# Performance work log

Measured on AMD Instinct MI355X. Metric: run time of the kernel, lower is better.

The kernel has to match this reference:

```python
import jax, jax.numpy as jnp
import numpy as np

EPS = 1e-6


def _layernorm2d(x, w, b):
    # Normalize over channel dim (axis=1) per pixel; x: [B,C,H,W]
    mu = jnp.mean(x, axis=1, keepdims=True)
    var = jnp.var(x, axis=1, keepdims=True)
    xn = (x - mu) * jax.lax.rsqrt(var + EPS)
    return xn * w[None, :, None, None] + b[None, :, None, None]


def _conv1x1(x, w, b):
    # 1x1 conv == channel matmul; w: [Cout, Cin], x: [B,Cin,H,W]
    return jnp.einsum('oc,bchw->bohw', w, x) + b[None, :, None, None]


def setup_inputs() -> dict:
    key = jax.random.key(0)
    ks = jax.random.split(key, 8)
    B, C, H, W = 4, 64, 180, 320
    s = C ** -0.5  # keep projection weights at sane scale
    return {
        'x_l': jax.random.normal(ks[0], (B, C, H, W), jnp.float32),
        'x_r': jax.random.normal(ks[1], (B, C, H, W), jnp.float32),
        'ln_l_w': jnp.ones((C,), jnp.float32),
        'ln_l_b': jnp.zeros((C,), jnp.float32),
        'ln_r_w': jnp.ones((C,), jnp.float32),
        'ln_r_b': jnp.zeros((C,), jnp.float32),
        'wq_l': jax.random.normal(ks[2], (C, C), jnp.float32) * s,
        'bq_l': jnp.zeros((C,), jnp.float32),
        'wq_r': jax.random.normal(ks[3], (C, C), jnp.float32) * s,
        'bq_r': jnp.zeros((C,), jnp.float32),
        'wv_l': jax.random.normal(ks[4], (C, C), jnp.float32) * s,
        'bv_l': jnp.zeros((C,), jnp.float32),
        'wv_r': jax.random.normal(ks[5], (C, C), jnp.float32) * s,
        'bv_r': jnp.zeros((C,), jnp.float32),
        'beta': jax.random.normal(ks[6], (C,), jnp.float32) * 0.1,
        'gamma': jax.random.normal(ks[7], (C,), jnp.float32) * 0.1,
    }


def reference(x_l, x_r, ln_l_w, ln_l_b, ln_r_w, ln_r_b,
              wq_l, bq_l, wq_r, bq_r, wv_l, bv_l, wv_r, bv_r,
              beta, gamma):
    C = x_l.shape[1]
    scale = C ** -0.5
    # Q projections of LayerNorm'd inputs (Select stub == identity pass-through)
    Q_l = _conv1x1(_layernorm2d(x_l, ln_l_w, ln_l_b), wq_l, bq_l)  # [B,C,H,W]
    Q_r = _conv1x1(_layernorm2d(x_r, ln_r_w, ln_r_b), wq_r, bq_r)  # [B,C,H,W]
    V_l = _conv1x1(x_l, wv_l, bv_l)  # [B,C,H,W]
    V_r = _conv1x1(x_r, wv_r, bv_r)  # [B,C,H,W]
    # attention over width per row: [B,H,Wl,Wr]
    attn = jnp.einsum('bchw,bchv->bhwv', Q_l, Q_r) * scale
    # r -> l: softmax over Wr (last axis), contract with V_r
    F_r2l = jnp.einsum('bhwv,bchv->bchw', jax.nn.softmax(attn, axis=-1), V_r)
    # l -> r: softmax over Wl (axis=2 of attn), contract with V_l
    F_l2r = jnp.einsum('bhwv,bchw->bchv', jax.nn.softmax(attn, axis=2), V_l)
    out_l = x_l + F_r2l * beta[None, :, None, None]
    out_r = x_r + F_l2r * gamma[None, :, None, None]
    return (out_l, out_r)
```

## Files before the change

### kernel.cpp

```cpp
#include <hip/hip_runtime.h>


#define HWs  57600
#define CHWs 3686400
#define TOTs 14745600
#define RST  72
#define VST  328
#define PTS  40

typedef short bf16x8 __attribute__((ext_vector_type(8)));
typedef float f32x4  __attribute__((ext_vector_type(4)));
union FragU { uint4 q; unsigned short u[8]; bf16x8 v; };

__device__ __forceinline__ unsigned short f2bf(float f) {
  unsigned u = __float_as_uint(f);
  u += 0x7fffu + ((u >> 16) & 1u);
  return (unsigned short)(u >> 16);
}
__device__ __forceinline__ float bf2f(unsigned short s) {
  return __uint_as_float(((unsigned)s) << 16);
}

__global__ __launch_bounds__(512, 2) void sfam_kernel(
    const float* __restrict__ x_l, const float* __restrict__ x_r,
    const float* __restrict__ ln_l_w, const float* __restrict__ ln_l_b,
    const float* __restrict__ ln_r_w, const float* __restrict__ ln_r_b,
    const float* __restrict__ wq_l, const float* __restrict__ bq_l,
    const float* __restrict__ wq_r, const float* __restrict__ bq_r,
    const float* __restrict__ wv_l, const float* __restrict__ bv_l,
    const float* __restrict__ wv_r, const float* __restrict__ bv_r,
    const float* __restrict__ beta, const float* __restrict__ gamma,
    float* __restrict__ out)
{
  __shared__ __align__(16) unsigned short Rs[320*RST];
  __shared__ __align__(16) unsigned short Ks[320*RST];
  __shared__ __align__(16) unsigned short Vb[64*VST];
  __shared__ __align__(16) unsigned short Pt[8*16*PTS];
  __shared__ float SR[8*320];
  __shared__ float MU[640], RSd[640];
  __shared__ float c_arr[320];
  __shared__ float BB[128];

  const int bh = blockIdx.x;
  const int b = bh / 180, h = bh - b*180;
  const int base = b*CHWs + h*320;

  const int t = threadIdx.x;
  const int wave = t >> 6, lane = t & 63;
  const int p = lane & 15, g = lane >> 4;
  const int nwt = (wave < 4) ? 3 : 2;
  const int w0 = (wave < 4) ? wave*48 : 192 + (wave-4)*32;

  for (int idx = t; idx < 1280; idx += 512) {
    int r2 = idx; const int side = (r2 >= 640); r2 -= side*640;
    const int half = (r2 >= 320); const int w = r2 - half*320;
    const int cb = half*32;
    const float* xp = side ? x_r : x_l;
    unsigned short* dst = side ? Ks : Rs;
    float s = 0.f, q = 0.f;
    #pragma unroll 8
    for (int c = 0; c < 32; ++c) {
      float v = xp[base + (cb+c)*HWs + w];
      s += v; q += v*v;
      dst[w*RST + cb + c] = f2bf(v);
    }
    SR[(side*2+half)*320 + w] = s;
    SR[(4+side*2+half)*320 + w] = q;
  }
  if (t < 128) {
    const int o = t & 63;
    const float* wqp = (t < 64) ? wq_l : wq_r;
    const float* lwp = (t < 64) ? ln_l_w : ln_r_w;
    const float* lbp = (t < 64) ? ln_l_b : ln_r_b;
    const float* bqp = (t < 64) ? bq_l : bq_r;
    float s = bqp[o];
    for (int c = 0; c < 64; ++c) s += wqp[o*64+c]*lwp[c]*lbp[c];
    BB[t] = s;
  }
  __syncthreads();
  for (int i = t; i < 640; i += 512) {
    const int side = (i >= 320); const int w = i - side*320;
    float m = (SR[(side*2)*320+w] + SR[(side*2+1)*320+w]) * (1.f/64.f);
    float q = (SR[(4+side*2)*320+w] + SR[(4+side*2+1)*320+w]) * (1.f/64.f) - m*m;
    MU[i] = m;
    RSd[i] = rsqrtf(q + 1e-6f);
  }
  __syncthreads();

  auto projV = [&](const float* wvp, const float* bvp, const unsigned short* src,
                   const float* mup, const float* rsp, bool inv) {
    bf16x8 bx[3][2];
    #pragma unroll
    for (int nt = 0; nt < 3; ++nt) if (nt < nwt) {
      const int w = w0 + nt*16 + p;
      const float mu = mup[w];
      const float sd = inv ? (1.0f / rsp[w]) : 0.f;
      #pragma unroll
      for (int kf = 0; kf < 2; ++kf) {
        FragU f; f.q = *(const uint4*)&src[w*RST + kf*32 + g*8];
        if (inv) {
          FragU rr;
          #pragma unroll
          for (int j = 0; j < 8; ++j) rr.u[j] = f2bf(bf2f(f.u[j])*sd + mu);
          bx[nt][kf] = rr.v;
        } else bx[nt][kf] = f.v;
      }
    }
    bf16x8 av[4][2];
    #pragma unroll
    for (int mt = 0; mt < 4; ++mt)
      #pragma unroll
      for (int kf = 0; kf < 2; ++kf) {
        FragU rr;
        #pragma unroll
        for (int j = 0; j < 8; ++j) rr.u[j] = f2bf(wvp[(mt*16+p)*64 + kf*32 + g*8 + j]);
        av[mt][kf] = rr.v;
      }
    f32x4 acc[4][3];
    #pragma unroll
    for (int mt = 0; mt < 4; ++mt)
      #pragma unroll
      for (int nt = 0; nt < 3; ++nt) acc[mt][nt] = (f32x4){0.f,0.f,0.f,0.f};
    #pragma unroll
    for (int mt = 0; mt < 4; ++mt)
      #pragma unroll
      for (int nt = 0; nt < 3; ++nt) if (nt < nwt)
        #pragma unroll
        for (int kf = 0; kf < 2; ++kf)
          acc[mt][nt] = __builtin_amdgcn_mfma_f32_16x16x32_bf16(av[mt][kf], bx[nt][kf], acc[mt][nt], 0,0,0);
    #pragma unroll
    for (int mt = 0; mt < 4; ++mt)
      #pragma unroll
      for (int nt = 0; nt < 3; ++nt) if (nt < nwt)
        #pragma unroll
        for (int r = 0; r < 4; ++r) {
          const int o = mt*16 + g*4 + r;
          Vb[o*VST + w0 + nt*16 + p] = f2bf(acc[mt][nt][r] + bvp[o]);
        }
  };

  projV(wv_l, bv_l, Rs, MU, RSd, false);

  float cR[3][4];
  {
    bf16x8 qa[3][2];
    #pragma unroll
    for (int wt = 0; wt < 3; ++wt) if (wt < nwt) {
      const int w = w0 + wt*16 + p;
      const float mu = MU[w], rs = RSd[w];
      #pragma unroll
      for (int kf = 0; kf < 2; ++kf) {
        FragU f; f.q = *(const uint4*)&Rs[w*RST + kf*32 + g*8];
        FragU rr;
        #pragma unroll
        for (int j = 0; j < 8; ++j) rr.u[j] = f2bf((bf2f(f.u[j]) - mu) * rs);
        qa[wt][kf] = rr.v;
      }
    }
    bf16x8 bw[4][2];
    #pragma unroll
    for (int ot = 0; ot < 4; ++ot)
      #pragma unroll
      for (int kf = 0; kf < 2; ++kf) {
        FragU rr;
        #pragma unroll
        for (int j = 0; j < 8; ++j) {
          const int c = kf*32 + g*8 + j;
          rr.u[j] = f2bf(wq_l[(ot*16+p)*64 + c] * ln_l_w[c]);
        }
        bw[ot][kf] = rr.v;
      }
    f32x4 qacc[3][4];
    #pragma unroll
    for (int wt = 0; wt < 3; ++wt)
      #pragma unroll
      for (int ot = 0; ot < 4; ++ot) qacc[wt][ot] = (f32x4){0.f,0.f,0.f,0.f};
    #pragma unroll
    for (int wt = 0; wt < 3; ++wt) if (wt < nwt)
      #pragma unroll
      for (int ot = 0; ot < 4; ++ot)
        #pragma unroll
        for (int kf = 0; kf < 2; ++kf)
          qacc[wt][ot] = __builtin_amdgcn_mfma_f32_16x16x32_bf16(qa[wt][kf], bw[ot][kf], qacc[wt][ot], 0,0,0);
    #pragma unroll
    for (int wt = 0; wt < 3; ++wt) {
      #pragma unroll
      for (int r = 0; r < 4; ++r) cR[wt][r] = 0.f;
      if (wt < nwt) {
        #pragma unroll
        for (int ot = 0; ot < 4; ++ot) {
          const float bl = BB[ot*16+p], br = BB[64 + ot*16+p];
          #pragma unroll
          for (int r = 0; r < 4; ++r) {
            const float qv = qacc[wt][ot][r] + bl;
            Rs[(w0 + wt*16 + g*4 + r)*RST + ot*16 + p] = f2bf(qv);
            cR[wt][r] += qv * br;
          }
        }
        #pragma unroll
        for (int r = 0; r < 4; ++r) {
          float cv = cR[wt][r];
          cv += __shfl_xor(cv, 1); cv += __shfl_xor(cv, 2);
          cv += __shfl_xor(cv, 4); cv += __shfl_xor(cv, 8);
          cv *= 0.125f;
          cR[wt][r] = cv;
          if (p == 0) c_arr[w0 + wt*16 + g*4 + r] = cv;
        }
      }
    }
  }

  {
    bf16x8 qla[3][2];
    #pragma unroll
    for (int wt = 0; wt < 3; ++wt) if (wt < nwt)
      #pragma unroll
      for (int kf = 0; kf < 2; ++kf) {
        FragU f; f.q = *(const uint4*)&Rs[(w0 + wt*16 + p)*RST + kf*32 + g*8];
        qla[wt][kf] = f.v;
      }
    bf16x8 bwt[4][2];
    #pragma unroll
    for (int ct = 0; ct < 4; ++ct) {
      const float lw = ln_r_w[ct*16 + p];
      #pragma unroll
      for (int kf = 0; kf < 2; ++kf) {
        FragU rr;
        #pragma unroll
        for (int j = 0; j < 8; ++j)
          rr.u[j] = f2bf(wq_r[(kf*32 + g*8 + j)*64 + ct*16 + p] * lw);
        bwt[ct][kf] = rr.v;
      }
    }
    f32x4 q2[3][4];
    #pragma unroll
    for (int wt = 0; wt < 3; ++wt)
      #pragma unroll
      for (int ct = 0; ct < 4; ++ct) q2[wt][ct] = (f32x4){0.f,0.f,0.f,0.f};
    #pragma unroll
    for (int wt = 0; wt < 3; ++wt) if (wt < nwt)
      #pragma unroll
      for (int ct = 0; ct < 4; ++ct)
        #pragma unroll
        for (int kf = 0; kf < 2; ++kf)
          q2[wt][ct] = __builtin_amdgcn_mfma_f32_16x16x32_bf16(qla[wt][kf], bwt[ct][kf], q2[wt][ct], 0,0,0);
    #pragma unroll
    for (int wt = 0; wt < 3; ++wt) if (wt < nwt)
      #pragma unroll
      for (int ct = 0; ct < 4; ++ct)
        #pragma unroll
        for (int r = 0; r < 4; ++r)
          Rs[(w0 + wt*16 + g*4 + r)*RST + ct*16 + p] = f2bf(q2[wt][ct][r] * 0.125f);
  }

  #pragma unroll
  for (int wt = 0; wt < 3; ++wt) if (wt < nwt) {
    const int w = w0 + wt*16 + p;
    const float mu = MU[320+w], rs = RSd[320+w];
    #pragma unroll
    for (int kf = 0; kf < 2; ++kf) {
      FragU f; f.q = *(const uint4*)&Ks[w*RST + kf*32 + g*8];
      FragU rr;
      #pragma unroll
      for (int j = 0; j < 8; ++j) rr.u[j] = f2bf((bf2f(f.u[j]) - mu) * rs);
      *(uint4*)&Ks[w*RST + kf*32 + g*8] = rr.q;
    }
  }
  __syncthreads();

  bf16x8 aq[3][2], ak[3][2];
  #pragma unroll
  for (int wt = 0; wt < 3; ++wt) if (wt < nwt)
    #pragma unroll
    for (int kf = 0; kf < 2; ++kf) {
      FragU f1; f1.q = *(const uint4*)&Rs[(w0 + wt*16 + p)*RST + kf*32 + g*8];
      aq[wt][kf] = f1.v;
      FragU f2; f2.q = *(const uint4*)&Ks[(w0 + wt*16 + p)*RST + kf*32 + g*8];
      ak[wt][kf] = f2.v;
    }

  float rm[3][4];
  #pragma unroll
  for (int wt = 0; wt < 3; ++wt)
    #pragma unroll
    for (int r = 0; r < 4; ++r) rm[wt][r] = -3.0e38f;
  for (int ch = 0; ch < 5; ++ch) {
    const int k0 = ch*64;
    bf16x8 bq[4][2];
    #pragma unroll
    for (int vt = 0; vt < 4; ++vt)
      #pragma unroll
      for (int kf = 0; kf < 2; ++kf) {
        FragU f; f.q = *(const uint4*)&Ks[(k0 + vt*16 + p)*RST + kf*32 + g*8];
        bq[vt][kf] = f.v;
      }
    f32x4 sacc[3][4];
    #pragma unroll
    for (int wt = 0; wt < 3; ++wt)
      #pragma unroll
      for (int vt = 0; vt < 4; ++vt) sacc[wt][vt] = (f32x4){0.f,0.f,0.f,0.f};
    #pragma unroll
    for (int wt = 0; wt < 3; ++wt) if (wt < nwt)
      #pragma unroll
      for (int vt = 0; vt < 4; ++vt)
        #pragma unroll
        for (int kf = 0; kf < 2; ++kf)
          sacc[wt][vt] = __builtin_amdgcn_mfma_f32_16x16x32_bf16(aq[wt][kf], bq[vt][kf], sacc[wt][vt], 0,0,0);
    #pragma unroll
    for (int wt = 0; wt < 3; ++wt) if (wt < nwt) {
      #pragma unroll
      for (int r = 0; r < 4; ++r) {
        float m4 = fmaxf(fmaxf(sacc[wt][0][r], sacc[wt][1][r]),
                         fmaxf(sacc[wt][2][r], sacc[wt][3][r])) + cR[wt][r];
        m4 = fmaxf(m4, __shfl_xor(m4, 1)); m4 = fmaxf(m4, __shfl_xor(m4, 2));
        m4 = fmaxf(m4, __shfl_xor(m4, 4)); m4 = fmaxf(m4, __shfl_xor(m4, 8));
        rm[wt][r] = fmaxf(rm[wt][r], m4);
      }
    }
    #pragma unroll
    for (int vt = 0; vt < 4; ++vt) {
      float cp = -3.0e38f;
      #pragma unroll
      for (int wt = 0; wt < 3; ++wt) if (wt < nwt)
        #pragma unroll
        for (int r = 0; r < 4; ++r) cp = fmaxf(cp, sacc[wt][vt][r] + cR[wt][r]);
      cp = fmaxf(cp, __shfl_xor(cp, 16));
      cp = fmaxf(cp, __shfl_xor(cp, 32));
      if (g == 0) SR[wave*320 + k0 + vt*16 + p] = cp;
    }
  }
  __syncthreads();
  if (t < 320) {
    float m = SR[t];
    #pragma unroll
    for (int j = 1; j < 8; ++j) m = fmaxf(m, SR[j*320 + t]);
    SR[t] = m;
  }
  __syncthreads();

  float ls[3][4];
  f32x4 oacc[3][4];
  auto attn_pass = [&](bf16x8 (&A)[3][2], const unsigned short* Bsrc,
                       float (&mx)[3][4], bool colc) {
    for (int ch = 0; ch < 5; ++ch) {
      const int k0 = ch*64;
      bf16x8 bq[4][2];
      #pragma unroll
      for (int vt = 0; vt < 4; ++vt)
        #pragma unroll
        for (int kf = 0; kf < 2; ++kf) {
          FragU f; f.q = *(const uint4*)&Bsrc[(k0 + vt*16 + p)*RST + kf*32 + g*8];
          bq[vt][kf] = f.v;
        }
      float cc4[4];
      #pragma unroll
      for (int vt = 0; vt < 4; ++vt) cc4[vt] = colc ? c_arr[k0 + vt*16 + p] : 0.f;
      f32x4 sacc[3][4];
      #pragma unroll
      for (int wt = 0; wt < 3; ++wt)
        #pragma unroll
        for (int vt = 0; vt < 4; ++vt) sacc[wt][vt] = (f32x4){0.f,0.f,0.f,0.f};
      #pragma unroll
      for (int wt = 0; wt < 3; ++wt) if (wt < nwt)
        #pragma unroll
        for (int vt = 0; vt < 4; ++vt)
          #pragma unroll
          for (int kf = 0; kf < 2; ++kf)
            sacc[wt][vt] = __builtin_amdgcn_mfma_f32_16x16x32_bf16(A[wt][kf], bq[vt][kf], sacc[wt][vt], 0,0,0);
      #pragma unroll
      for (int wt = 0; wt < 3; ++wt) if (wt < nwt) {
        #pragma unroll
        for (int r = 0; r < 4; ++r) {
          const float rc = colc ? 0.f : cR[wt][r];
          float rsum = 0.f;
          #pragma unroll
          for (int vt = 0; vt < 4; ++vt) {
            const float e = __expf(sacc[wt][vt][r] + rc + cc4[vt] - mx[wt][r]);
            sacc[wt][vt][r] = e; rsum += e;
          }
          rsum += __shfl_xor(rsum, 1); rsum += __shfl_xor(rsum, 2);
          rsum += __shfl_xor(rsum, 4); rsum += __shfl_xor(rsum, 8);
          ls[wt][r] += rsum;
        }
      }
      bf16x8 bvv[2][4];
      #pragma unroll
      for (int kf = 0; kf < 2; ++kf)
        #pragma unroll
        for (int ot = 0; ot < 4; ++ot) {
          FragU f; f.q = *(const uint4*)&Vb[(ot*16+p)*VST + k0 + kf*32 + g*8];
          bvv[kf][ot] = f.v;
        }
      unsigned short* ptw = &Pt[wave*16*PTS];
      #pragma unroll
      for (int wt = 0; wt < 3; ++wt) if (wt < nwt) {
        #pragma unroll
        for (int kf = 0; kf < 2; ++kf) {
          #pragma unroll
          for (int vh = 0; vh < 2; ++vh) {
            const int vt2 = kf*2 + vh;
            #pragma unroll
            for (int r = 0; r < 4; ++r)
              ptw[(g*4 + r)*PTS + vh*16 + p] = f2bf(sacc[wt][vt2][r]);
          }
          FragU fa; fa.q = *(const uint4*)&ptw[p*PTS + g*8];
          #pragma unroll
          for (int ot = 0; ot < 4; ++ot)
            oacc[wt][ot] = __builtin_amdgcn_mfma_f32_16x16x32_bf16(fa.v, bvv[kf][ot], oacc[wt][ot], 0,0,0);
        }
      }
    }
  };

  float cmR[3][4];
  #pragma unroll
  for (int wt = 0; wt < 3; ++wt)
    #pragma unroll
    for (int r = 0; r < 4; ++r) {
      cmR[wt][r] = (wt < nwt) ? SR[w0 + wt*16 + g*4 + r] : 0.f;
      ls[wt][r] = 0.f;
    }
  #pragma unroll
  for (int wt = 0; wt < 3; ++wt)
    #pragma unroll
    for (int ot = 0; ot < 4; ++ot) oacc[wt][ot] = (f32x4){0.f,0.f,0.f,0.f};
  attn_pass(ak, Rs, cmR, true);
  __syncthreads();

  #pragma unroll
  for (int wt = 0; wt < 3; ++wt) if (wt < nwt)
    #pragma unroll
    for (int r = 0; r < 4; ++r) {
      const float inv = 1.0f / ls[wt][r];
      #pragma unroll
      for (int ot = 0; ot < 4; ++ot)
        Rs[(w0 + wt*16 + g*4 + r)*RST + ot*16 + p] = f2bf(oacc[wt][ot][r] * inv);
    }

  projV(wv_r, bv_r, Ks, MU+320, RSd+320, true);
  __syncthreads();

  #pragma unroll
  for (int wt = 0; wt < 3; ++wt)
    #pragma unroll
    for (int r = 0; r < 4; ++r) ls[wt][r] = 0.f;
  #pragma unroll
  for (int wt = 0; wt < 3; ++wt)
    #pragma unroll
    for (int ot = 0; ot < 4; ++ot) oacc[wt][ot] = (f32x4){0.f,0.f,0.f,0.f};
  attn_pass(aq, Ks, rm, false);
  __syncthreads();

  #pragma unroll
  for (int wt = 0; wt < 3; ++wt) if (wt < nwt)
    #pragma unroll
    for (int r = 0; r < 4; ++r) {
      const float inv = 1.0f / ls[wt][r];
      #pragma unroll
      for (int ot = 0; ot < 4; ++ot)
        Ks[(w0 + wt*16 + g*4 + r)*RST + ot*16 + p] = f2bf(oacc[wt][ot][r] * inv);
    }
  __syncthreads();

  for (int idx = t; idx < 1280; idx += 512) {
    int r2 = idx; const int side = (r2 >= 640); r2 -= side*640;
    const int half = (r2 >= 320); const int w = r2 - half*320;
    const int cb = half*32;
    const float* xs = side ? x_r : x_l;
    const unsigned short* Osrc = side ? Rs : Ks;
    const float* sc = side ? gamma : beta;
    float* op = out + (side ? TOTs : 0);
    #pragma unroll 8
    for (int c = 0; c < 32; ++c) {
      const int cc = cb + c;
      const int gi = base + cc*HWs + w;
      op[gi] = xs[gi] + sc[cc] * bf2f(Osrc[w*RST + cc]);
    }
  }
}

extern "C" void kernel_launch(void* const* d_in, const int* in_sizes, int n_in,
                              void* d_out, int out_size, void* d_ws, size_t ws_size,
                              hipStream_t stream) {
  (void)in_sizes; (void)n_in; (void)d_ws; (void)ws_size; (void)out_size;
  sfam_kernel<<<dim3(720), dim3(512), 0, stream>>>(
      (const float*)d_in[0],  (const float*)d_in[1],
      (const float*)d_in[2],  (const float*)d_in[3],
      (const float*)d_in[4],  (const float*)d_in[5],
      (const float*)d_in[6],  (const float*)d_in[7],
      (const float*)d_in[8],  (const float*)d_in[9],
      (const float*)d_in[10], (const float*)d_in[11],
      (const float*)d_in[12], (const float*)d_in[13],
      (const float*)d_in[14], (const float*)d_in[15],
      (float*)d_out);
}
```

Baseline: 434.1 us.

## Double block to 1024 threads and use atomic column-max reduction

Launches 16 waves per block instead of 8, reassigning width tiles so the first four waves take two 16-wide tiles and the rest take one. The cross-wave column-max now uses atomicMax on order-preserving encoded floats in shared memory, replacing the staging array and its extra reduction pass and barrier. LayerNorm statistics are computed in one pass per pixel over all 64 channels, with 16-byte vectorized shared-memory stores and loads. The per-wave P staging stride shrinks to 36 so the bigger buffer fits, which leaves the 16-byte fragment reads only 8-byte aligned; the 1024-thread bound also caps registers per thread and may cause spills.

```diff
diff --git a/kernel.cpp b/kernel.cpp
--- a/kernel.cpp
+++ b/kernel.cpp
@@ -6,7 +6,7 @@
 #define TOTs 14745600
 #define RST  72
 #define VST  328
-#define PTS  40
+#define PTS  36
 
 typedef short bf16x8 __attribute__((ext_vector_type(8)));
 typedef float f32x4  __attribute__((ext_vector_type(4)));
@@ -20,8 +20,15 @@
 __device__ __forceinline__ float bf2f(unsigned short s) {
   return __uint_as_float(((unsigned)s) << 16);
 }
-
-__global__ __launch_bounds__(512, 2) void sfam_kernel(
+__device__ __forceinline__ unsigned fenc(float f) {
+  unsigned u = __float_as_uint(f);
+  return u ^ (0x80000000u | (unsigned)(-(int)(u >> 31)));
+}
+__device__ __forceinline__ float fdec(unsigned k) {
+  return __uint_as_float(k ^ (0x80000000u | (unsigned)(-(int)((k >> 31) ^ 1u))));
+}
+
+__global__ __launch_bounds__(1024) void sfam_kernel(
     const float* __restrict__ x_l, const float* __restrict__ x_r,
     const float* __restrict__ ln_l_w, const float* __restrict__ ln_l_b,
     const float* __restrict__ ln_r_w, const float* __restrict__ ln_r_b,
@@ -35,8 +42,8 @@
   __shared__ __align__(16) unsigned short Rs[320*RST];
   __shared__ __align__(16) unsigned short Ks[320*RST];
   __shared__ __align__(16) unsigned short Vb[64*VST];
-  __shared__ __align__(16) unsigned short Pt[8*16*PTS];
-  __shared__ float SR[8*320];
+  __shared__ __align__(16) unsigned short Pt[16*16*PTS];
+  __shared__ unsigned CMu[320];
   __shared__ float MU[640], RSd[640];
   __shared__ float c_arr[320];
   __shared__ float BB[128];
@@ -48,25 +55,32 @@
   const int t = threadIdx.x;
   const int wave = t >> 6, lane = t & 63;
   const int p = lane & 15, g = lane >> 4;
-  const int nwt = (wave < 4) ? 3 : 2;
-  const int w0 = (wave < 4) ? wave*48 : 192 + (wave-4)*32;
-
-  for (int idx = t; idx < 1280; idx += 512) {
-    int r2 = idx; const int side = (r2 >= 640); r2 -= side*640;
-    const int half = (r2 >= 320); const int w = r2 - half*320;
-    const int cb = half*32;
+  const int nwt = (wave < 4) ? 2 : 1;
+  const int w0 = (wave < 4) ? wave*32 : 128 + (wave-4)*16;
+
+  for (int w2 = t; w2 < 640; w2 += 1024) {
+    const int side = (w2 >= 320);
+    const int w = w2 - side*320;
     const float* xp = side ? x_r : x_l;
     unsigned short* dst = side ? Ks : Rs;
-    float s = 0.f, q = 0.f;
-    #pragma unroll 8
-    for (int c = 0; c < 32; ++c) {
-      float v = xp[base + (cb+c)*HWs + w];
-      s += v; q += v*v;
-      dst[w*RST + cb + c] = f2bf(v);
-    }
-    SR[(side*2+half)*320 + w] = s;
-    SR[(4+side*2+half)*320 + w] = q;
-  }
+    float s0 = 0.f, q0 = 0.f, s1 = 0.f, q1 = 0.f;
+    #pragma unroll
+    for (int cb = 0; cb < 64; cb += 8) {
+      FragU f;
+      #pragma unroll
+      for (int j = 0; j < 8; ++j) {
+        const float v = xp[base + (cb+j)*HWs + w];
+        if (cb < 32) { s0 += v; q0 += v*v; } else { s1 += v; q1 += v*v; }
+        f.u[j] = f2bf(v);
+      }
+      *(uint4*)&dst[w*RST + cb] = f.q;
+    }
+    const float m  = (s0 + s1) * (1.f/64.f);
+    const float vv = (q0 + q1) * (1.f/64.f) - m*m;
+    MU[side*320 + w]  = m;
+    RSd[side*320 + w] = rsqrtf(vv + 1e-6f);
+  }
+  if (t < 320) CMu[t] = 0u;
   if (t < 128) {
     const int o = t & 63;
     const float* wqp = (t < 64) ? wq_l : wq_r;
@@ -78,20 +92,12 @@
     BB[t] = s;
   }
   __syncthreads();
-  for (int i = t; i < 640; i += 512) {
-    const int side = (i >= 320); const int w = i - side*320;
-    float m = (SR[(side*2)*320+w] + SR[(side*2+1)*320+w]) * (1.f/64.f);
-    float q = (SR[(4+side*2)*320+w] + SR[(4+side*2+1)*320+w]) * (1.f/64.f) - m*m;
-    MU[i] = m;
-    RSd[i] = rsqrtf(q + 1e-6f);
-  }
-  __syncthreads();
 
   auto projV = [&](const float* wvp, const float* bvp, const unsigned short* src,
                    const float* mup, const float* rsp, bool inv) {
-    bf16x8 bx[3][2];
-    #pragma unroll
-    for (int nt = 0; nt < 3; ++nt) if (nt < nwt) {
+    bf16x8 bx[2][2];
+    #pragma unroll
+    for (int nt = 0; nt < 2; ++nt) if (nt < nwt) {
       const int w = w0 + nt*16 + p;
       const float mu = mup[w];
       const float sd = inv ? (1.0f / rsp[w]) : 0.f;
@@ -116,22 +122,22 @@
         for (int j = 0; j < 8; ++j) rr.u[j] = f2bf(wvp[(mt*16+p)*64 + kf*32 + g*8 + j]);
         av[mt][kf] = rr.v;
       }
-    f32x4 acc[4][3];
+    f32x4 acc[4][2];
     #pragma unroll
     for (int mt = 0; mt < 4; ++mt)
       #pragma unroll
-      for (int nt = 0; nt < 3; ++nt) acc[mt][nt] = (f32x4){0.f,0.f,0.f,0.f};
+      for (int nt = 0; nt < 2; ++nt) acc[mt][nt] = (f32x4){0.f,0.f,0.f,0.f};
     #pragma unroll
     for (int mt = 0; mt < 4; ++mt)
       #pragma unroll
-      for (int nt = 0; nt < 3; ++nt) if (nt < nwt)
+      for (int nt = 0; nt < 2; ++nt) if (nt < nwt)
         #pragma unroll
         for (int kf = 0; kf < 2; ++kf)
           acc[mt][nt] = __builtin_amdgcn_mfma_f32_16x16x32_bf16(av[mt][kf], bx[nt][kf], acc[mt][nt], 0,0,0);
     #pragma unroll
     for (int mt = 0; mt < 4; ++mt)
       #pragma unroll
-      for (int nt = 0; nt < 3; ++nt) if (nt < nwt)
+      for (int nt = 0; nt < 2; ++nt) if (nt < nwt)
         #pragma unroll
         for (int r = 0; r < 4; ++r) {
           const int o = mt*16 + g*4 + r;
@@ -141,11 +147,11 @@
 
   projV(wv_l, bv_l, Rs, MU, RSd, false);
 
-  float cR[3][4];
+  float cR[2][4];
   {
-    bf16x8 qa[3][2];
-    #pragma unroll
-    for (int wt = 0; wt < 3; ++wt) if (wt < nwt) {
+    bf16x8 qa[2][2];
+    #pragma unroll
+    for (int wt = 0; wt < 2; ++wt) if (wt < nwt) {
       const int w = w0 + wt*16 + p;
       const float mu = MU[w], rs = RSd[w];
       #pragma unroll
@@ -170,20 +176,20 @@
         }
         bw[ot][kf] = rr.v;
       }
-    f32x4 qacc[3][4];
-    #pragma unroll
-    for (int wt = 0; wt < 3; ++wt)
+    f32x4 qacc[2][4];
+    #pragma unroll
+    for (int wt = 0; wt < 2; ++wt)
       #pragma unroll
       for (int ot = 0; ot < 4; ++ot) qacc[wt][ot] = (f32x4){0.f,0.f,0.f,0.f};
     #pragma unroll
-    for (int wt = 0; wt < 3; ++wt) if (wt < nwt)
+    for (int wt = 0; wt < 2; ++wt) if (wt < nwt)
       #pragma unroll
       for (int ot = 0; ot < 4; ++ot)
         #pragma unroll
         for (int kf = 0; kf < 2; ++kf)
           qacc[wt][ot] = __builtin_amdgcn_mfma_f32_16x16x32_bf16(qa[wt][kf], bw[ot][kf], qacc[wt][ot], 0,0,0);
     #pragma unroll
-    for (int wt = 0; wt < 3; ++wt) {
+    for (int wt = 0; wt < 2; ++wt) {
       #pragma unroll
       for (int r = 0; r < 4; ++r) cR[wt][r] = 0.f;
       if (wt < nwt) {
@@ -211,9 +217,9 @@
   }
 
   {
-    bf16x8 qla[3][2];
-    #pragma unroll
-    for (int wt = 0; wt < 3; ++wt) if (wt < nwt)
+    bf16x8 qla[2][2];
+    #pragma unroll
+    for (int wt = 0; wt < 2; ++wt) if (wt < nwt)
       #pragma unroll
       for (int kf = 0; kf < 2; ++kf) {
         FragU f; f.q = *(const uint4*)&Rs[(w0 + wt*16 + p)*RST + kf*32 + g*8];
@@ -232,20 +238,20 @@
         bwt[ct][kf] = rr.v;
       }
     }
-    f32x4 q2[3][4];
-    #pragma unroll
-    for (int wt = 0; wt < 3; ++wt)
+    f32x4 q2[2][4];
+    #pragma unroll
+    for (int wt = 0; wt < 2; ++wt)
       #pragma unroll
       for (int ct = 0; ct < 4; ++ct) q2[wt][ct] = (f32x4){0.f,0.f,0.f,0.f};
     #pragma unroll
-    for (int wt = 0; wt < 3; ++wt) if (wt < nwt)
+    for (int wt = 0; wt < 2; ++wt) if (wt < nwt)
       #pragma unroll
       for (int ct = 0; ct < 4; ++ct)
         #pragma unroll
         for (int kf = 0; kf < 2; ++kf)
           q2[wt][ct] = __builtin_amdgcn_mfma_f32_16x16x32_bf16(qla[wt][kf], bwt[ct][kf], q2[wt][ct], 0,0,0);
     #pragma unroll
-    for (int wt = 0; wt < 3; ++wt) if (wt < nwt)
+    for (int wt = 0; wt < 2; ++wt) if (wt < nwt)
       #pragma unroll
       for (int ct = 0; ct < 4; ++ct)
         #pragma unroll
@@ -254,7 +260,7 @@
   }
 
   #pragma unroll
-  for (int wt = 0; wt < 3; ++wt) if (wt < nwt) {
+  for (int wt = 0; wt < 2; ++wt) if (wt < nwt) {
     const int w = w0 + wt*16 + p;
     const float mu = MU[320+w], rs = RSd[320+w];
     #pragma unroll
@@ -268,9 +274,9 @@
   }
   __syncthreads();
 
-  bf16x8 aq[3][2], ak[3][2];
-  #pragma unroll
-  for (int wt = 0; wt < 3; ++wt) if (wt < nwt)
+  bf16x8 aq[2][2], ak[2][2];
+  #pragma unroll
+  for (int wt = 0; wt < 2; ++wt) if (wt < nwt)
     #pragma unroll
     for (int kf = 0; kf < 2; ++kf) {
       FragU f1; f1.q = *(const uint4*)&Rs[(w0 + wt*16 + p)*RST + kf*32 + g*8];
@@ -279,9 +285,9 @@
       ak[wt][kf] = f2.v;
     }
 
-  float rm[3][4];
-  #pragma unroll
-  for (int wt = 0; wt < 3; ++wt)
+  float rm[2][4];
+  #pragma unroll
+  for (int wt = 0; wt < 2; ++wt)
     #pragma unroll
     for (int r = 0; r < 4; ++r) rm[wt][r] = -3.0e38f;
   for (int ch = 0; ch < 5; ++ch) {
@@ -294,20 +300,20 @@
         FragU f; f.q = *(const uint4*)&Ks[(k0 + vt*16 + p)*RST + kf*32 + g*8];
         bq[vt][kf] = f.v;
       }
-    f32x4 sacc[3][4];
-    #pragma unroll
-    for (int wt = 0; wt < 3; ++wt)
+    f32x4 sacc[2][4];
+    #pragma unroll
+    for (int wt = 0; wt < 2; ++wt)
       #pragma unroll
       for (int vt = 0; vt < 4; ++vt) sacc[wt][vt] = (f32x4){0.f,0.f,0.f,0.f};
     #pragma unroll
-    for (int wt = 0; wt < 3; ++wt) if (wt < nwt)
+    for (int wt = 0; wt < 2; ++wt) if (wt < nwt)
       #pragma unroll
       for (int vt = 0; vt < 4; ++vt)
         #pragma unroll
         for (int kf = 0; kf < 2; ++kf)
           sacc[wt][vt] = __builtin_amdgcn_mfma_f32_16x16x32_bf16(aq[wt][kf], bq[vt][kf], sacc[wt][vt], 0,0,0);
     #pragma unroll
-    for (int wt = 0; wt < 3; ++wt) if (wt < nwt) {
+    for (int wt = 0; wt < 2; ++wt) if (wt < nwt) {
       #pragma unroll
       for (int r = 0; r < 4; ++r) {
         float m4 = fmaxf(fmaxf(sacc[wt][0][r], sacc[wt][1][r]),
@@ -321,27 +327,20 @@
     for (int vt = 0; vt < 4; ++vt) {
       float cp = -3.0e38f;
       #pragma unroll
-      for (int wt = 0; wt < 3; ++wt) if (wt < nwt)
+      for (int wt = 0; wt < 2; ++wt) if (wt < nwt)
         #pragma unroll
         for (int r = 0; r < 4; ++r) cp = fmaxf(cp, sacc[wt][vt][r] + cR[wt][r]);
       cp = fmaxf(cp, __shfl_xor(cp, 16));
       cp = fmaxf(cp, __shfl_xor(cp, 32));
-      if (g == 0) SR[wave*320 + k0 + vt*16 + p] = cp;
-    }
-  }
-  __syncthreads();
-  if (t < 320) {
-    float m = SR[t];
-    #pragma unroll
-    for (int j = 1; j < 8; ++j) m = fmaxf(m, SR[j*320 + t]);
-    SR[t] = m;
-  }
-  __syncthreads();
-
-  float ls[3][4];
-  f32x4 oacc[3][4];
-  auto attn_pass = [&](bf16x8 (&A)[3][2], const unsigned short* Bsrc,
-                       float (&mx)[3][4], bool colc) {
+      if (g == 0) atomicMax(&CMu[k0 + vt*16 + p], fenc(cp));
+    }
+  }
+  __syncthreads();
+
+  float ls[2][4];
+  f32x4 oacc[2][4];
+  auto attn_pass = [&](bf16x8 (&A)[2][2], const unsigned short* Bsrc,
+                       float (&mx)[2][4], bool colc) {
     for (int ch = 0; ch < 5; ++ch) {
       const int k0 = ch*64;
       bf16x8 bq[4][2];
@@ -355,20 +354,20 @@
       float cc4[4];
       #pragma unroll
       for (int vt = 0; vt < 4; ++vt) cc4[vt] = colc ? c_arr[k0 + vt*16 + p] : 0.f;
-      f32x4 sacc[3][4];
-      #pragma unroll
-      for (int wt = 0; wt < 3; ++wt)
+      f32x4 sacc[2][4];
+      #pragma unroll
+      for (int wt = 0; wt < 2; ++wt)
         #pragma unroll
         for (int vt = 0; vt < 4; ++vt) sacc[wt][vt] = (f32x4){0.f,0.f,0.f,0.f};
       #pragma unroll
-      for (int wt = 0; wt < 3; ++wt) if (wt < nwt)
+      for (int wt = 0; wt < 2; ++wt) if (wt < nwt)
         #pragma unroll
         for (int vt = 0; vt < 4; ++vt)
           #pragma unroll
           for (int kf = 0; kf < 2; ++kf)
             sacc[wt][vt] = __builtin_amdgcn_mfma_f32_16x16x32_bf16(A[wt][kf], bq[vt][kf], sacc[wt][vt], 0,0,0);
       #pragma unroll
-      for (int wt = 0; wt < 3; ++wt) if (wt < nwt) {
+      for (int wt = 0; wt < 2; ++wt) if (wt < nwt) {
         #pragma unroll
         for (int r = 0; r < 4; ++r) {
           const float rc = colc ? 0.f : cR[wt][r];
@@ -393,7 +392,7 @@
         }
       unsigned short* ptw = &Pt[wave*16*PTS];
       #pragma unroll
-      for (int wt = 0; wt < 3; ++wt) if (wt < nwt) {
+      for (int wt = 0; wt < 2; ++wt) if (wt < nwt) {
         #pragma unroll
         for (int kf = 0; kf < 2; ++kf) {
           #pragma unroll
@@ -412,23 +411,23 @@
     }
   };
 
-  float cmR[3][4];
-  #pragma unroll
-  for (int wt = 0; wt < 3; ++wt)
+  float cmR[2][4];
+  #pragma unroll
+  for (int wt = 0; wt < 2; ++wt)
     #pragma unroll
     for (int r = 0; r < 4; ++r) {
-      cmR[wt][r] = (wt < nwt) ? SR[w0 + wt*16 + g*4 + r] : 0.f;
+      cmR[wt][r] = (wt < nwt) ? fdec(CMu[w0 + wt*16 + g*4 + r]) : 0.f;
       ls[wt][r] = 0.f;
     }
   #pragma unroll
-  for (int wt = 0; wt < 3; ++wt)
+  for (int wt = 0; wt < 2; ++wt)
     #pragma unroll
     for (int ot = 0; ot < 4; ++ot) oacc[wt][ot] = (f32x4){0.f,0.f,0.f,0.f};
   attn_pass(ak, Rs, cmR, true);
   __syncthreads();
 
   #pragma unroll
-  for (int wt = 0; wt < 3; ++wt) if (wt < nwt)
+  for (int wt = 0; wt < 2; ++wt) if (wt < nwt)
     #pragma unroll
     for (int r = 0; r < 4; ++r) {
       const float inv = 1.0f / ls[wt][r];
@@ -441,18 +440,18 @@
   __syncthreads();
 
   #pragma unroll
-  for (int wt = 0; wt < 3; ++wt)
+  for (int wt = 0; wt < 2; ++wt)
     #pragma unroll
     for (int r = 0; r < 4; ++r) ls[wt][r] = 0.f;
   #pragma unroll
-  for (int wt = 0; wt < 3; ++wt)
+  for (int wt = 0; wt < 2; ++wt)
     #pragma unroll
     for (int ot = 0; ot < 4; ++ot) oacc[wt][ot] = (f32x4){0.f,0.f,0.f,0.f};
   attn_pass(aq, Ks, rm, false);
   __syncthreads();
 
   #pragma unroll
-  for (int wt = 0; wt < 3; ++wt) if (wt < nwt)
+  for (int wt = 0; wt < 2; ++wt) if (wt < nwt)
     #pragma unroll
     for (int r = 0; r < 4; ++r) {
       const float inv = 1.0f / ls[wt][r];
@@ -462,19 +461,22 @@
     }
   __syncthreads();
 
-  for (int idx = t; idx < 1280; idx += 512) {
-    int r2 = idx; const int side = (r2 >= 640); r2 -= side*640;
-    const int half = (r2 >= 320); const int w = r2 - half*320;
-    const int cb = half*32;
+  for (int w2 = t; w2 < 640; w2 += 1024) {
+    const int side = (w2 >= 320);
+    const int w = w2 - side*320;
     const float* xs = side ? x_r : x_l;
     const unsigned short* Osrc = side ? Rs : Ks;
     const float* sc = side ? gamma : beta;
     float* op = out + (side ? TOTs : 0);
-    #pragma unroll 8
-    for (int c = 0; c < 32; ++c) {
-      const int cc = cb + c;
-      const int gi = base + cc*HWs + w;
-      op[gi] = xs[gi] + sc[cc] * bf2f(Osrc[w*RST + cc]);
+    #pragma unroll
+    for (int cb = 0; cb < 64; cb += 8) {
+      FragU f; f.q = *(const uint4*)&Osrc[w*RST + cb];
+      #pragma unroll
+      for (int j = 0; j < 8; ++j) {
+        const int cc = cb + j;
+        const int gi = base + cc*HWs + w;
+        op[gi] = xs[gi] + sc[cc] * bf2f(f.u[j]);
+      }
     }
   }
 }
@@ -483,7 +485,7 @@
                               void* d_out, int out_size, void* d_ws, size_t ws_size,
                               hipStream_t stream) {
   (void)in_sizes; (void)n_in; (void)d_ws; (void)ws_size; (void)out_size;
-  sfam_kernel<<<dim3(720), dim3(512), 0, stream>>>(
+  sfam_kernel<<<dim3(720), dim3(1024), 0, stream>>>(
       (const float*)d_in[0],  (const float*)d_in[1],
       (const float*)d_in[2],  (const float*)d_in[3],
       (const float*)d_in[4],  (const float*)d_in[5],
```

Result: slower. 507.9 us (+17.0%).
